# Kernel tuning notes

Hardware: AMD Instinct MI355X
Metric: run time of the kernel (lower is better)

## Reference

```python
import jax, jax.numpy as jnp
import numpy as np

N_ENT = 50000
N_REL2 = 100   # num_relations * 2
N_BASES = 16
DIM = 64
N_EDGES = 100000


def _rgcn_conv(x, edge_index, edge_type, edge_norm, basis, att, root, bias):
    # x: [N, D]; basis: [B, D, D]; att: [R, B]; root: [D, D]; bias: [D]
    src = edge_index[0]
    dst = edge_index[1]
    num_nodes = x.shape[0]
    # Per-edge relation weight is w[edge_type] with w = att @ basis (reshaped).
    # By linearity we contract x_j with each basis first, then mix with the
    # per-edge attention coefficients -- same math, avoids the [E, D, D] gather.
    coeff = att[edge_type]                          # [E, B]
    xb = jnp.einsum('ei,bio->ebo', x[src], basis)   # [E, B, D]
    msg = jnp.einsum('eb,ebo->eo', coeff, xb)       # [E, D]
    msg = msg * edge_norm[:, None]
    # scatter-mean aggregation at target nodes
    s = jax.ops.segment_sum(msg, dst, num_segments=num_nodes)
    cnt = jax.ops.segment_sum(jnp.ones((msg.shape[0],), msg.dtype), dst,
                              num_segments=num_nodes)
    agg = s / jnp.maximum(cnt, 1.0)[:, None]
    # root transform + bias
    return agg + x @ root + bias


def setup_inputs() -> dict:
    key = jax.random.key(0)
    ks = jax.random.split(key, 12)
    E = N_EDGES
    inp = {
        'entity': jnp.arange(N_ENT, dtype=jnp.int64) if jax.config.jax_enable_x64 else jnp.arange(N_ENT, dtype=jnp.int32),
        'edge_index': jax.random.randint(ks[0], (2, E), 0, N_ENT),
        'edge_type': jax.random.randint(ks[1], (E,), 0, N_REL2),
        'edge_norm': jax.random.uniform(ks[2], (E,), dtype=jnp.float32),
        'emb': jax.random.normal(ks[3], (N_ENT, DIM), dtype=jnp.float32) * 0.1,
        'basis1': jax.random.normal(ks[4], (N_BASES, DIM, DIM), dtype=jnp.float32) * 0.05,
        'att1': jax.random.normal(ks[5], (N_REL2, N_BASES), dtype=jnp.float32) * 0.1,
        'root1': jax.random.normal(ks[6], (DIM, DIM), dtype=jnp.float32) * 0.05,
        'bias1': jnp.zeros((DIM,), dtype=jnp.float32),
        'basis2': jax.random.normal(ks[7], (N_BASES, DIM, DIM), dtype=jnp.float32) * 0.05,
        'att2': jax.random.normal(ks[8], (N_REL2, N_BASES), dtype=jnp.float32) * 0.1,
        'root2': jax.random.normal(ks[9], (DIM, DIM), dtype=jnp.float32) * 0.05,
        'bias2': jnp.zeros((DIM,), dtype=jnp.float32),
    }
    return inp


def reference(entity, edge_index, edge_type, edge_norm, emb,
              basis1, att1, root1, bias1, basis2, att2, root2, bias2):
    x = emb[entity]                                  # embedding lookup [N, D]
    x = _rgcn_conv(x, edge_index, edge_type, edge_norm, basis1, att1, root1, bias1)
    x = _rgcn_conv(x, edge_index, edge_type, edge_norm, basis2, att2, root2, bias2)
    return x
```

## Files before the change

kernel.cpp:

```cpp
#include <hip/hip_runtime.h>

#define NN 50000
#define NR 100
#define NB 16
#define D  64
#define NE 100000

#define HB  196
#define EPB 512
#define ZB  196
#define GB  ((NN * 16 + 255) / 256)

#define CHUNK 128
#define GROUPS 2
#define EGRID 1024

#define NPB 128
#define NGRID ((NN + NPB - 1) / NPB)

typedef float f32x4  __attribute__((ext_vector_type(4)));
typedef short bf16x8 __attribute__((ext_vector_type(8)));

__device__ __forceinline__ short f2bf(float f) {
    unsigned u = __float_as_uint(f);
    return (short)((u + 0x7FFFu + ((u >> 16) & 1u)) >> 16);
}

__device__ __forceinline__ bf16x8 pack8(f32x4 a, f32x4 b) {
    bf16x8 t;
    t[0] = f2bf(a.x); t[1] = f2bf(a.y); t[2] = f2bf(a.z); t[3] = f2bf(a.w);
    t[4] = f2bf(b.x); t[5] = f2bf(b.y); t[6] = f2bf(b.z); t[7] = f2bf(b.w);
    return t;
}

__global__ __launch_bounds__(256) void prep_all(
    const float* __restrict__ att1, const float* __restrict__ basis1,
    const float* __restrict__ root1,
    const float* __restrict__ att2, const float* __restrict__ basis2,
    const float* __restrict__ root2,
    const int* __restrict__ entity, const f32x4* __restrict__ emb4,
    float* __restrict__ Wt1, float* __restrict__ Wt2,
    float* __restrict__ rT1, float* __restrict__ rT2,
    f32x4* __restrict__ x04, int* __restrict__ deg, int* __restrict__ nodeCur)
{
    __shared__ float t[64 * 65];
    int b = blockIdx.x;
    if (b < 2 * NR) {
        int layer = b >= NR;
        int r = layer ? b - NR : b;
        const float* att   = layer ? att2 : att1;
        const float* basis = layer ? basis2 : basis1;
        float*       Wt    = layer ? Wt2 : Wt1;
        float a[NB];
#pragma unroll
        for (int bb = 0; bb < NB; ++bb) a[bb] = att[r * NB + bb];
#pragma unroll
        for (int i = 0; i < 16; ++i) {
            int idx = i * 256 + threadIdx.x;
            float acc = 0.f;
#pragma unroll
            for (int bb = 0; bb < NB; ++bb) acc += a[bb] * basis[bb * 4096 + idx];
            t[(idx >> 6) * 65 + (idx & 63)] = acc;
        }
        __syncthreads();
#pragma unroll
        for (int i = 0; i < 16; ++i) {
            int j = i * 256 + threadIdx.x;
            Wt[(size_t)r * 4096 + j] = t[(j & 63) * 65 + (j >> 6)];
        }
    } else if (b < 2 * NR + 2) {
        const float* root = (b == 2 * NR) ? root1 : root2;
        float*       rT   = (b == 2 * NR) ? rT1 : rT2;
#pragma unroll
        for (int i = 0; i < 16; ++i) {
            int idx = i * 256 + threadIdx.x;
            t[(idx >> 6) * 65 + (idx & 63)] = root[idx];
        }
        __syncthreads();
#pragma unroll
        for (int i = 0; i < 16; ++i) {
            int j = i * 256 + threadIdx.x;
            rT[j] = t[(j & 63) * 65 + (j >> 6)];
        }
    } else if (b < 2 * NR + 2 + ZB) {
        int i = (b - (2 * NR + 2)) * 256 + threadIdx.x;
        deg[i] = 0; nodeCur[i] = 0;
    } else {
        int idx = (b - (2 * NR + 2 + ZB)) * 256 + threadIdx.x;
        if (idx < NN * 16) {
            int n = idx >> 4;
            int q = idx & 15;
            x04[idx] = emb4[(size_t)entity[n] * 16 + q];
        }
    }
}

__global__ __launch_bounds__(256) void hist_edges(
    const int* __restrict__ et, const int* __restrict__ dst,
    int* __restrict__ blockHist, int* __restrict__ deg)
{
    __shared__ int lh[NR];
    for (int i = threadIdx.x; i < NR; i += 256) lh[i] = 0;
    __syncthreads();
#pragma unroll
    for (int i = 0; i < EPB / 256; ++i) {
        int e = blockIdx.x * EPB + i * 256 + threadIdx.x;
        if (e < NE) {
            atomicAdd(&lh[et[e]], 1);
            atomicAdd(&deg[dst[e]], 1);
        }
    }
    __syncthreads();
    for (int i = threadIdx.x; i < NR; i += 256)
        blockHist[blockIdx.x * NR + i] = lh[i];
}

__global__ __launch_bounds__(256) void scans(
    const int* __restrict__ blockHist, int* __restrict__ blockPrefix,
    int* __restrict__ relTot, const int* __restrict__ deg,
    int* __restrict__ nodePre, int* __restrict__ blockSumN)
{
    __shared__ int sc[256];
    int t = threadIdx.x;
    if (blockIdx.x < NR) {
        int r = blockIdx.x;
        int v = (t < HB) ? blockHist[t * NR + r] : 0;
        sc[t] = v;
        __syncthreads();
#pragma unroll
        for (int off = 1; off < 256; off <<= 1) {
            int a = (t >= off) ? sc[t - off] : 0;
            __syncthreads();
            sc[t] += a;
            __syncthreads();
        }
        if (t < HB) blockPrefix[t * NR + r] = sc[t] - v;
        if (t == 0) relTot[r] = sc[255];
    } else {
        int b = blockIdx.x - NR;
        int n = b * 256 + t;
        int v = deg[n];
        sc[t] = v;
        __syncthreads();
#pragma unroll
        for (int off = 1; off < 256; off <<= 1) {
            int a = (t >= off) ? sc[t - off] : 0;
            __syncthreads();
            sc[t] += a;
            __syncthreads();
        }
        nodePre[n] = sc[t] - v;
        if (t == 255) blockSumN[b] = sc[255];
    }
}

__global__ __launch_bounds__(256) void scanK(
    const int* __restrict__ relTot, const int* __restrict__ blockSumN,
    int* __restrict__ offs, int* __restrict__ nbG,
    int* __restrict__ tabR, int* __restrict__ tabS,
    int* __restrict__ nodeBlockBase)
{
    __shared__ int totL[NR];
    __shared__ int offL[NR + 1];
    __shared__ int cnbL[NR + 1];
    __shared__ int sc2[256];
    int t = threadIdx.x;
    if (t < NR) totL[t] = relTot[t];
    int v2 = (t < ZB) ? blockSumN[t] : 0;
    sc2[t] = v2;
    __syncthreads();
    if (t == 0) {
        int off = 0, cb = 0;
        for (int r = 0; r < NR; ++r) {
            offL[r] = off; cnbL[r] = cb;
            off += totL[r];
            cb  += (totL[r] + CHUNK - 1) / CHUNK;
        }
        offL[NR] = off; cnbL[NR] = cb;
    }
    __syncthreads();
#pragma unroll
    for (int off = 1; off < 256; off <<= 1) {
        int a = (t >= off) ? sc2[t - off] : 0;
        __syncthreads();
        sc2[t] += a;
        __syncthreads();
    }
    if (t < ZB) nodeBlockBase[t] = sc2[t] - v2;
    if (t == 0) nodeBlockBase[ZB] = sc2[255];
    if (t <= NR) offs[t] = offL[t];
    if (t == 0) nbG[0] = cnbL[NR];
    int nb = cnbL[NR];
    for (int e = t; e < nb; e += 256) {
        int lo = 0, hi = NR;
        while (hi - lo > 1) { int mid = (lo + hi) >> 1; if (cnbL[mid] <= e) lo = mid; else hi = mid; }
        tabR[e] = lo;
        tabS[e] = offL[lo] + (e - cnbL[lo]) * CHUNK;
    }
}

__global__ __launch_bounds__(256) void scatter2(
    const int* __restrict__ src, const int* __restrict__ dst,
    const int* __restrict__ et, const float* __restrict__ en,
    const int* __restrict__ offs, const int* __restrict__ blockPrefix,
    const int* __restrict__ nodePre, const int* __restrict__ nodeBlockBase,
    int* __restrict__ nodeCur, int* __restrict__ srcS,
    float* __restrict__ normS, int* __restrict__ dstIdx)
{
    __shared__ int lcur[NR];
    for (int i = threadIdx.x; i < NR; i += 256)
        lcur[i] = offs[i] + blockPrefix[blockIdx.x * NR + i];
    __syncthreads();
#pragma unroll
    for (int i = 0; i < EPB / 256; ++i) {
        int e = blockIdx.x * EPB + i * 256 + threadIdx.x;
        if (e < NE) {
            int r = et[e];
            int p = atomicAdd(&lcur[r], 1);
            srcS[p] = src[e]; normS[p] = en[e];
            int n = dst[e];
            int q = nodeBlockBase[n >> 8] + nodePre[n] + atomicAdd(&nodeCur[n], 1);
            dstIdx[q] = p;
        }
    }
}

__global__ __launch_bounds__(256, 4) void edge_mfma(
    const int* __restrict__ srcS, const float* __restrict__ normS,
    const int* __restrict__ offs, const int* __restrict__ tabR,
    const int* __restrict__ tabS, const int* __restrict__ nbG,
    const float* __restrict__ x, const float* __restrict__ Wt,
    float* __restrict__ msg)
{
    __shared__ float LW[64 * 68];
    int b = blockIdx.x;
    if (b >= nbG[0]) return;
    int r  = tabR[b];
    int cs = tabS[b];
    int tid = threadIdx.x;

    {
        const f32x4* __restrict__ Wg = (const f32x4*)(Wt + (size_t)r * 4096);
#pragma unroll
        for (int i = 0; i < 4; ++i) {
            int v = tid + i * 256;
            int d = v >> 4, k4 = v & 15;
            *(f32x4*)(LW + d * 68 + k4 * 4) = Wg[v];
        }
    }
    __syncthreads();

    int lane = tid & 63, wid = tid >> 6;
    int c15 = lane & 15, kg = lane >> 4;

    bf16x8 B[4][2];
#pragma unroll
    for (int nt = 0; nt < 4; ++nt)
#pragma unroll
        for (int ks = 0; ks < 2; ++ks) {
            const f32x4* p = (const f32x4*)(LW + (nt * 16 + c15) * 68 + ks * 32 + kg * 8);
            B[nt][ks] = pack8(p[0], p[1]);
        }

    int segE = offs[r + 1];
    int bend = cs + CHUNK < segE ? cs + CHUNK : segE;

#pragma unroll 1
    for (int g = 0; g < GROUPS; ++g) {
        int gs = cs + wid * (GROUPS * 16) + g * 16;
        if (gs >= bend) break;
        int ge = gs + 16 < bend ? gs + 16 : bend;

        int e  = gs + c15;
        int ec = e < ge ? e : ge - 1;
        float nrm = (e < ge) ? normS[ec] : 0.f;
        int   sn  = srcS[ec];

        const f32x4* xr  = (const f32x4*)(x + (size_t)sn * 64 + kg * 8);
        const f32x4* xr2 = (const f32x4*)(x + (size_t)sn * 64 + 32 + kg * 8);
        bf16x8 A0 = pack8(xr[0]  * nrm, xr[1]  * nrm);
        bf16x8 A1 = pack8(xr2[0] * nrm, xr2[1] * nrm);

        f32x4 z = {0.f, 0.f, 0.f, 0.f};
        f32x4 acc[4] = {z, z, z, z};
#pragma unroll
        for (int nt = 0; nt < 4; ++nt) {
            acc[nt] = __builtin_amdgcn_mfma_f32_16x16x32_bf16(A0, B[nt][0], acc[nt], 0, 0, 0);
            acc[nt] = __builtin_amdgcn_mfma_f32_16x16x32_bf16(A1, B[nt][1], acc[nt], 0, 0, 0);
        }
#pragma unroll
        for (int nt = 0; nt < 4; ++nt)
#pragma unroll
            for (int j = 0; j < 4; ++j) {
                int er = gs + kg * 4 + j;
                if (er < ge)
                    msg[(size_t)er * 64 + nt * 16 + c15] = acc[nt][j];
            }
    }
}

__global__ __launch_bounds__(256) void agg_mean(
    const float* __restrict__ msg, const int* __restrict__ dstIdx,
    const int* __restrict__ nodePre, const int* __restrict__ nodeBB,
    float* __restrict__ agg)
{
    int n    = blockIdx.x * 4 + (threadIdx.x >> 6);
    int lane = threadIdx.x & 63;
    if (n >= NN) return;
    int blk  = n >> 8;
    int base = nodeBB[blk];
    int lo = base + nodePre[n];
    int hi = ((n & 255) == 255) ? nodeBB[blk + 1] : base + nodePre[n + 1];
    float acc = 0.f;
    for (int q = lo; q < hi; ++q)
        acc += msg[(size_t)dstIdx[q] * 64 + lane];
    float c = (float)(hi - lo);
    c = c > 1.f ? c : 1.f;
    agg[(size_t)n * 64 + lane] = acc / c;
}

__global__ __launch_bounds__(256, 4) void node_mfma(
    const float* __restrict__ x, const float* __restrict__ agg,
    const float* __restrict__ rT, const float* __restrict__ bias,
    float* __restrict__ out)
{
    __shared__ float LW[64 * 68];
    int tid = threadIdx.x;
    {
        const f32x4* __restrict__ Rg = (const f32x4*)rT;
#pragma unroll
        for (int i = 0; i < 4; ++i) {
            int v = tid + i * 256;
            int d = v >> 4, k4 = v & 15;
            *(f32x4*)(LW + d * 68 + k4 * 4) = Rg[v];
        }
    }
    __syncthreads();

    int lane = tid & 63, wid = tid >> 6;
    int c15 = lane & 15, kg = lane >> 4;

    bf16x8 B[4][2];
#pragma unroll
    for (int nt = 0; nt < 4; ++nt)
#pragma unroll
        for (int ks = 0; ks < 2; ++ks) {
            const f32x4* p = (const f32x4*)(LW + (nt * 16 + c15) * 68 + ks * 32 + kg * 8);
            B[nt][ks] = pack8(p[0], p[1]);
        }
    float bv[4];
#pragma unroll
    for (int nt = 0; nt < 4; ++nt) bv[nt] = bias[nt * 16 + c15];

#pragma unroll 1
    for (int g = 0; g < GROUPS; ++g) {
        int gs = blockIdx.x * NPB + wid * (GROUPS * 16) + g * 16;
        if (gs >= NN) break;
        int ge = gs + 16 < NN ? gs + 16 : NN;

        int n  = gs + c15;
        int nc = n < ge ? n : ge - 1;
        const f32x4* xr  = (const f32x4*)(x + (size_t)nc * 64 + kg * 8);
        const f32x4* xr2 = (const f32x4*)(x + (size_t)nc * 64 + 32 + kg * 8);
        bf16x8 A0 = pack8(xr[0], xr[1]);
        bf16x8 A1 = pack8(xr2[0], xr2[1]);

        f32x4 z = {0.f, 0.f, 0.f, 0.f};
        f32x4 acc[4] = {z, z, z, z};
#pragma unroll
        for (int nt = 0; nt < 4; ++nt) {
            acc[nt] = __builtin_amdgcn_mfma_f32_16x16x32_bf16(A0, B[nt][0], acc[nt], 0, 0, 0);
            acc[nt] = __builtin_amdgcn_mfma_f32_16x16x32_bf16(A1, B[nt][1], acc[nt], 0, 0, 0);
        }
#pragma unroll
        for (int nt = 0; nt < 4; ++nt)
#pragma unroll
            for (int j = 0; j < 4; ++j) {
                int nr = gs + kg * 4 + j;
                if (nr < ge) {
                    size_t off = (size_t)nr * 64 + nt * 16 + c15;
                    out[off] = agg[off] + acc[nt][j] + bv[nt];
                }
            }
    }
}

extern "C" void kernel_launch(void* const* d_in, const int* in_sizes, int n_in,
                              void* d_out, int out_size, void* d_ws, size_t ws_size,
                              hipStream_t stream) {
    const int*   entity    = (const int*)d_in[0];
    const int*   edge_index= (const int*)d_in[1];
    const int*   edge_type = (const int*)d_in[2];
    const float* edge_norm = (const float*)d_in[3];
    const float* emb       = (const float*)d_in[4];
    const float* basis1    = (const float*)d_in[5];
    const float* att1      = (const float*)d_in[6];
    const float* root1     = (const float*)d_in[7];
    const float* bias1     = (const float*)d_in[8];
    const float* basis2    = (const float*)d_in[9];
    const float* att2      = (const float*)d_in[10];
    const float* root2     = (const float*)d_in[11];
    const float* bias2     = (const float*)d_in[12];

    const int* src = edge_index;
    const int* dst = edge_index + NE;

    float* ws    = (float*)d_ws;
    float* Wt1   = ws;
    float* Wt2   = Wt1 + (size_t)NR * 4096;
    float* rT1   = Wt2 + (size_t)NR * 4096;
    float* rT2   = rT1 + 4096;
    float* x0    = rT2 + 4096;
    float* msg   = x0  + (size_t)NN * D;
    float* agg   = msg + (size_t)NE * D;
    float* normS = agg + (size_t)NN * D;
    int*   offs        = (int*)(normS + NE);
    int*   relTot      = offs + NR + 3;
    int*   nbG         = relTot + NR;
    int*   blockHist   = nbG + 3;
    int*   blockPrefix = blockHist + HB * NR;
    int*   tabR        = blockPrefix + HB * NR;
    int*   tabS        = tabR + EGRID;
    int*   srcS        = tabS + EGRID;
    int*   deg         = srcS + NE;
    int*   nodePre     = deg + ZB * 256;
    int*   nodeCur     = nodePre + ZB * 256;
    int*   blockSumN   = nodeCur + ZB * 256;
    int*   nodeBB      = blockSumN + ZB + 4;
    int*   dstIdx      = nodeBB + ZB + 5;

    float* out = (float*)d_out;

    prep_all<<<2 * NR + 2 + ZB + GB, 256, 0, stream>>>(
        att1, basis1, root1, att2, basis2, root2,
        entity, (const f32x4*)emb, Wt1, Wt2, rT1, rT2,
        (f32x4*)x0, deg, nodeCur);
    hist_edges<<<HB, 256, 0, stream>>>(edge_type, dst, blockHist, deg);
    scans<<<NR + ZB, 256, 0, stream>>>(blockHist, blockPrefix, relTot,
                                       deg, nodePre, blockSumN);
    scanK<<<1, 256, 0, stream>>>(relTot, blockSumN, offs, nbG, tabR, tabS, nodeBB);
    scatter2<<<HB, 256, 0, stream>>>(src, dst, edge_type, edge_norm,
                                     offs, blockPrefix, nodePre, nodeBB,
                                     nodeCur, srcS, normS, dstIdx);

    edge_mfma<<<EGRID, 256, 0, stream>>>(srcS, normS, offs, tabR, tabS, nbG,
                                         x0, Wt1, msg);
    agg_mean<<<(NN + 3) / 4, 256, 0, stream>>>(msg, dstIdx, nodePre, nodeBB, agg);
    node_mfma<<<NGRID, 256, 0, stream>>>(x0, agg, rT1, bias1, out);

    edge_mfma<<<EGRID, 256, 0, stream>>>(srcS, normS, offs, tabR, tabS, nbG,
                                         out, Wt2, msg);
    agg_mean<<<(NN + 3) / 4, 256, 0, stream>>>(msg, dstIdx, nodePre, nodeBB, agg);
    node_mfma<<<NGRID, 256, 0, stream>>>(out, agg, rT2, bias2, out);
}
```

Baseline: 128.5 us.

## Pad relation segments to 16, load weights per wave, fuse aggregation with node transform

Each relation's edge segment is padded to a multiple of 16 with zero-norm dummy edges, and a per-edge relation id array is stored. Every 16-edge MFMA group therefore has a single relation, which removes the chunk lookup tables. The edge kernel reads the relation id per group and loads its weights straight from global memory into registers, dropping the LDS staging and block barrier. The mean aggregation and root-transform kernels are merged into one agg_node kernel per layer, cutting two launches. The cost is padded msg rows plus repeated global weight reads per wave that hit L2.

```diff
diff --git a/kernel.cpp b/kernel.cpp
--- a/kernel.cpp
+++ b/kernel.cpp
@@ -5,18 +5,19 @@
 #define NB 16
 #define D  64
 #define NE 100000
+#define NE2 (NE + 16 * NR)
 
 #define HB  196
 #define EPB 512
 #define ZB  196
 #define GB  ((NN * 16 + 255) / 256)
 
-#define CHUNK 128
 #define GROUPS 2
-#define EGRID 1024
-
-#define NPB 128
-#define NGRID ((NN + NPB - 1) / NPB)
+#define EPBK (64 * GROUPS)
+#define EGRID ((NE2 + EPBK - 1) / EPBK)
+
+#define NPBK 64
+#define NGRID ((NN + NPBK - 1) / NPBK)
 
 typedef float f32x4  __attribute__((ext_vector_type(4)));
 typedef short bf16x8 __attribute__((ext_vector_type(8)));
@@ -156,13 +157,11 @@
 
 __global__ __launch_bounds__(256) void scanK(
     const int* __restrict__ relTot, const int* __restrict__ blockSumN,
-    int* __restrict__ offs, int* __restrict__ nbG,
-    int* __restrict__ tabR, int* __restrict__ tabS,
-    int* __restrict__ nodeBlockBase)
+    int* __restrict__ offs, int* __restrict__ nbG, int* __restrict__ nodeBB,
+    int* __restrict__ srcS, float* __restrict__ normS, int* __restrict__ rS)
 {
     __shared__ int totL[NR];
     __shared__ int offL[NR + 1];
-    __shared__ int cnbL[NR + 1];
     __shared__ int sc2[256];
     int t = threadIdx.x;
     if (t < NR) totL[t] = relTot[t];
@@ -170,13 +169,12 @@
     sc2[t] = v2;
     __syncthreads();
     if (t == 0) {
-        int off = 0, cb = 0;
+        int off = 0;
         for (int r = 0; r < NR; ++r) {
-            offL[r] = off; cnbL[r] = cb;
-            off += totL[r];
-            cb  += (totL[r] + CHUNK - 1) / CHUNK;
-        }
-        offL[NR] = off; cnbL[NR] = cb;
+            offL[r] = off;
+            off = (off + totL[r] + 15) & ~15;
+        }
+        offL[NR] = off;
     }
     __syncthreads();
 #pragma unroll
@@ -186,16 +184,13 @@
         sc2[t] += a;
         __syncthreads();
     }
-    if (t < ZB) nodeBlockBase[t] = sc2[t] - v2;
-    if (t == 0) nodeBlockBase[ZB] = sc2[255];
+    if (t < ZB) nodeBB[t] = sc2[t] - v2;
+    if (t == 0) nodeBB[ZB] = sc2[255];
     if (t <= NR) offs[t] = offL[t];
-    if (t == 0) nbG[0] = cnbL[NR];
-    int nb = cnbL[NR];
-    for (int e = t; e < nb; e += 256) {
-        int lo = 0, hi = NR;
-        while (hi - lo > 1) { int mid = (lo + hi) >> 1; if (cnbL[mid] <= e) lo = mid; else hi = mid; }
-        tabR[e] = lo;
-        tabS[e] = offL[lo] + (e - cnbL[lo]) * CHUNK;
+    if (t == 0) nbG[0] = offL[NR];
+    if (t < NR) {
+        int g0 = offL[t] + totL[t], g1 = offL[t + 1];
+        for (int p = g0; p < g1; ++p) { srcS[p] = 0; normS[p] = 0.f; rS[p] = t; }
     }
 }
 
@@ -205,7 +200,7 @@
     const int* __restrict__ offs, const int* __restrict__ blockPrefix,
     const int* __restrict__ nodePre, const int* __restrict__ nodeBlockBase,
     int* __restrict__ nodeCur, int* __restrict__ srcS,
-    float* __restrict__ normS, int* __restrict__ dstIdx)
+    float* __restrict__ normS, int* __restrict__ rS, int* __restrict__ dstIdx)
 {
     __shared__ int lcur[NR];
     for (int i = threadIdx.x; i < NR; i += 256)
@@ -217,7 +212,7 @@
         if (e < NE) {
             int r = et[e];
             int p = atomicAdd(&lcur[r], 1);
-            srcS[p] = src[e]; normS[p] = en[e];
+            srcS[p] = src[e]; normS[p] = en[e]; rS[p] = r;
             int n = dst[e];
             int q = nodeBlockBase[n >> 8] + nodePre[n] + atomicAdd(&nodeCur[n], 1);
             dstIdx[q] = p;
@@ -225,57 +220,38 @@
     }
 }
 
-__global__ __launch_bounds__(256, 4) void edge_mfma(
+__global__ __launch_bounds__(256) void edge_mfma(
     const int* __restrict__ srcS, const float* __restrict__ normS,
-    const int* __restrict__ offs, const int* __restrict__ tabR,
-    const int* __restrict__ tabS, const int* __restrict__ nbG,
+    const int* __restrict__ rS, const int* __restrict__ nbG,
     const float* __restrict__ x, const float* __restrict__ Wt,
     float* __restrict__ msg)
 {
-    __shared__ float LW[64 * 68];
-    int b = blockIdx.x;
-    if (b >= nbG[0]) return;
-    int r  = tabR[b];
-    int cs = tabS[b];
     int tid = threadIdx.x;
-
-    {
-        const f32x4* __restrict__ Wg = (const f32x4*)(Wt + (size_t)r * 4096);
-#pragma unroll
-        for (int i = 0; i < 4; ++i) {
-            int v = tid + i * 256;
-            int d = v >> 4, k4 = v & 15;
-            *(f32x4*)(LW + d * 68 + k4 * 4) = Wg[v];
-        }
-    }
-    __syncthreads();
-
     int lane = tid & 63, wid = tid >> 6;
     int c15 = lane & 15, kg = lane >> 4;
-
+    int padTot = nbG[0];
+    int rcur = -1;
     bf16x8 B[4][2];
-#pragma unroll
-    for (int nt = 0; nt < 4; ++nt)
-#pragma unroll
-        for (int ks = 0; ks < 2; ++ks) {
-            const f32x4* p = (const f32x4*)(LW + (nt * 16 + c15) * 68 + ks * 32 + kg * 8);
-            B[nt][ks] = pack8(p[0], p[1]);
-        }
-
-    int segE = offs[r + 1];
-    int bend = cs + CHUNK < segE ? cs + CHUNK : segE;
 
 #pragma unroll 1
     for (int g = 0; g < GROUPS; ++g) {
-        int gs = cs + wid * (GROUPS * 16) + g * 16;
-        if (gs >= bend) break;
-        int ge = gs + 16 < bend ? gs + 16 : bend;
-
+        int gs = blockIdx.x * EPBK + wid * (16 * GROUPS) + g * 16;
+        if (gs >= padTot) break;
+        int r = __builtin_amdgcn_readfirstlane(rS[gs]);
+        if (r != rcur) {
+            rcur = r;
+            const float* __restrict__ Wr = Wt + (size_t)r * 4096;
+#pragma unroll
+            for (int nt = 0; nt < 4; ++nt)
+#pragma unroll
+                for (int ks = 0; ks < 2; ++ks) {
+                    const f32x4* p = (const f32x4*)(Wr + (nt * 16 + c15) * 64 + ks * 32 + kg * 8);
+                    B[nt][ks] = pack8(p[0], p[1]);
+                }
+        }
         int e  = gs + c15;
-        int ec = e < ge ? e : ge - 1;
-        float nrm = (e < ge) ? normS[ec] : 0.f;
-        int   sn  = srcS[ec];
-
+        float nrm = normS[e];
+        int   sn  = srcS[e];
         const f32x4* xr  = (const f32x4*)(x + (size_t)sn * 64 + kg * 8);
         const f32x4* xr2 = (const f32x4*)(x + (size_t)sn * 64 + 32 + kg * 8);
         bf16x8 A0 = pack8(xr[0]  * nrm, xr[1]  * nrm);
@@ -291,98 +267,79 @@
 #pragma unroll
         for (int nt = 0; nt < 4; ++nt)
 #pragma unroll
-            for (int j = 0; j < 4; ++j) {
-                int er = gs + kg * 4 + j;
-                if (er < ge)
-                    msg[(size_t)er * 64 + nt * 16 + c15] = acc[nt][j];
-            }
-    }
-}
-
-__global__ __launch_bounds__(256) void agg_mean(
-    const float* __restrict__ msg, const int* __restrict__ dstIdx,
-    const int* __restrict__ nodePre, const int* __restrict__ nodeBB,
-    float* __restrict__ agg)
-{
-    int n    = blockIdx.x * 4 + (threadIdx.x >> 6);
-    int lane = threadIdx.x & 63;
-    if (n >= NN) return;
-    int blk  = n >> 8;
-    int base = nodeBB[blk];
-    int lo = base + nodePre[n];
-    int hi = ((n & 255) == 255) ? nodeBB[blk + 1] : base + nodePre[n + 1];
-    float acc = 0.f;
-    for (int q = lo; q < hi; ++q)
-        acc += msg[(size_t)dstIdx[q] * 64 + lane];
-    float c = (float)(hi - lo);
-    c = c > 1.f ? c : 1.f;
-    agg[(size_t)n * 64 + lane] = acc / c;
-}
-
-__global__ __launch_bounds__(256, 4) void node_mfma(
-    const float* __restrict__ x, const float* __restrict__ agg,
-    const float* __restrict__ rT, const float* __restrict__ bias,
+            for (int j = 0; j < 4; ++j)
+                msg[(size_t)(gs + kg * 4 + j) * 64 + nt * 16 + c15] = acc[nt][j];
+    }
+}
+
+__global__ __launch_bounds__(256) void agg_node(
+    const float* __restrict__ x, const float* __restrict__ msg,
+    const int* __restrict__ dstIdx, const int* __restrict__ nodePre,
+    const int* __restrict__ nodeBB, const float* __restrict__ rT,
+    const float* __restrict__ bias, float* __restrict__ agg,
     float* __restrict__ out)
 {
-    __shared__ float LW[64 * 68];
     int tid = threadIdx.x;
-    {
-        const f32x4* __restrict__ Rg = (const f32x4*)rT;
-#pragma unroll
-        for (int i = 0; i < 4; ++i) {
-            int v = tid + i * 256;
-            int d = v >> 4, k4 = v & 15;
-            *(f32x4*)(LW + d * 68 + k4 * 4) = Rg[v];
-        }
-    }
-    __syncthreads();
-
     int lane = tid & 63, wid = tid >> 6;
     int c15 = lane & 15, kg = lane >> 4;
+    int wbase = blockIdx.x * NPBK + wid * 16;
+
+#pragma unroll 1
+    for (int ln = 0; ln < 16; ++ln) {
+        int n = wbase + ln;
+        if (n >= NN) break;
+        int blk  = n >> 8;
+        int base = nodeBB[blk];
+        int lo = base + nodePre[n];
+        int hi = ((n & 255) == 255) ? nodeBB[blk + 1] : base + nodePre[n + 1];
+        float acc = 0.f;
+        for (int q = lo; q < hi; ++q)
+            acc += msg[(size_t)dstIdx[q] * 64 + lane];
+        float c = (float)(hi - lo);
+        c = c > 1.f ? c : 1.f;
+        agg[(size_t)n * 64 + lane] = acc / c;
+    }
+    __syncthreads();
+
+    if (wbase >= NN) return;
+    int ge = wbase + 16 < NN ? wbase + 16 : NN;
 
     bf16x8 B[4][2];
 #pragma unroll
     for (int nt = 0; nt < 4; ++nt)
 #pragma unroll
         for (int ks = 0; ks < 2; ++ks) {
-            const f32x4* p = (const f32x4*)(LW + (nt * 16 + c15) * 68 + ks * 32 + kg * 8);
+            const f32x4* p = (const f32x4*)(rT + (nt * 16 + c15) * 64 + ks * 32 + kg * 8);
             B[nt][ks] = pack8(p[0], p[1]);
         }
     float bv[4];
 #pragma unroll
     for (int nt = 0; nt < 4; ++nt) bv[nt] = bias[nt * 16 + c15];
 
-#pragma unroll 1
-    for (int g = 0; g < GROUPS; ++g) {
-        int gs = blockIdx.x * NPB + wid * (GROUPS * 16) + g * 16;
-        if (gs >= NN) break;
-        int ge = gs + 16 < NN ? gs + 16 : NN;
-
-        int n  = gs + c15;
-        int nc = n < ge ? n : ge - 1;
-        const f32x4* xr  = (const f32x4*)(x + (size_t)nc * 64 + kg * 8);
-        const f32x4* xr2 = (const f32x4*)(x + (size_t)nc * 64 + 32 + kg * 8);
-        bf16x8 A0 = pack8(xr[0], xr[1]);
-        bf16x8 A1 = pack8(xr2[0], xr2[1]);
-
-        f32x4 z = {0.f, 0.f, 0.f, 0.f};
-        f32x4 acc[4] = {z, z, z, z};
-#pragma unroll
-        for (int nt = 0; nt < 4; ++nt) {
-            acc[nt] = __builtin_amdgcn_mfma_f32_16x16x32_bf16(A0, B[nt][0], acc[nt], 0, 0, 0);
-            acc[nt] = __builtin_amdgcn_mfma_f32_16x16x32_bf16(A1, B[nt][1], acc[nt], 0, 0, 0);
-        }
-#pragma unroll
-        for (int nt = 0; nt < 4; ++nt)
-#pragma unroll
-            for (int j = 0; j < 4; ++j) {
-                int nr = gs + kg * 4 + j;
-                if (nr < ge) {
-                    size_t off = (size_t)nr * 64 + nt * 16 + c15;
-                    out[off] = agg[off] + acc[nt][j] + bv[nt];
-                }
+    int n  = wbase + c15;
+    int nc = n < ge ? n : ge - 1;
+    const f32x4* xr  = (const f32x4*)(x + (size_t)nc * 64 + kg * 8);
+    const f32x4* xr2 = (const f32x4*)(x + (size_t)nc * 64 + 32 + kg * 8);
+    bf16x8 A0 = pack8(xr[0], xr[1]);
+    bf16x8 A1 = pack8(xr2[0], xr2[1]);
+
+    f32x4 z = {0.f, 0.f, 0.f, 0.f};
+    f32x4 acc[4] = {z, z, z, z};
+#pragma unroll
+    for (int nt = 0; nt < 4; ++nt) {
+        acc[nt] = __builtin_amdgcn_mfma_f32_16x16x32_bf16(A0, B[nt][0], acc[nt], 0, 0, 0);
+        acc[nt] = __builtin_amdgcn_mfma_f32_16x16x32_bf16(A1, B[nt][1], acc[nt], 0, 0, 0);
+    }
+#pragma unroll
+    for (int nt = 0; nt < 4; ++nt)
+#pragma unroll
+        for (int j = 0; j < 4; ++j) {
+            int nr = wbase + kg * 4 + j;
+            if (nr < ge) {
+                size_t off = (size_t)nr * 64 + nt * 16 + c15;
+                out[off] = agg[off] + acc[nt][j] + bv[nt];
             }
-    }
+        }
 }
 
 extern "C" void kernel_launch(void* const* d_in, const int* in_sizes, int n_in,
@@ -412,17 +369,16 @@
     float* rT2   = rT1 + 4096;
     float* x0    = rT2 + 4096;
     float* msg   = x0  + (size_t)NN * D;
-    float* agg   = msg + (size_t)NE * D;
+    float* agg   = msg + (size_t)NE2 * D;
     float* normS = agg + (size_t)NN * D;
-    int*   offs        = (int*)(normS + NE);
+    int*   offs        = (int*)(normS + NE2);
     int*   relTot      = offs + NR + 3;
     int*   nbG         = relTot + NR;
     int*   blockHist   = nbG + 3;
     int*   blockPrefix = blockHist + HB * NR;
-    int*   tabR        = blockPrefix + HB * NR;
-    int*   tabS        = tabR + EGRID;
-    int*   srcS        = tabS + EGRID;
-    int*   deg         = srcS + NE;
+    int*   srcS        = blockPrefix + HB * NR;
+    int*   rS          = srcS + NE2;
+    int*   deg         = rS + NE2;
     int*   nodePre     = deg + ZB * 256;
     int*   nodeCur     = nodePre + ZB * 256;
     int*   blockSumN   = nodeCur + ZB * 256;
@@ -438,18 +394,17 @@
     hist_edges<<<HB, 256, 0, stream>>>(edge_type, dst, blockHist, deg);
     scans<<<NR + ZB, 256, 0, stream>>>(blockHist, blockPrefix, relTot,
                                        deg, nodePre, blockSumN);
-    scanK<<<1, 256, 0, stream>>>(relTot, blockSumN, offs, nbG, tabR, tabS, nodeBB);
+    scanK<<<1, 256, 0, stream>>>(relTot, blockSumN, offs, nbG, nodeBB,
+                                 srcS, normS, rS);
     scatter2<<<HB, 256, 0, stream>>>(src, dst, edge_type, edge_norm,
                                      offs, blockPrefix, nodePre, nodeBB,
-                                     nodeCur, srcS, normS, dstIdx);
-
-    edge_mfma<<<EGRID, 256, 0, stream>>>(srcS, normS, offs, tabR, tabS, nbG,
-                                         x0, Wt1, msg);
-    agg_mean<<<(NN + 3) / 4, 256, 0, stream>>>(msg, dstIdx, nodePre, nodeBB, agg);
-    node_mfma<<<NGRID, 256, 0, stream>>>(x0, agg, rT1, bias1, out);
-
-    edge_mfma<<<EGRID, 256, 0, stream>>>(srcS, normS, offs, tabR, tabS, nbG,
-                                         out, Wt2, msg);
-    agg_mean<<<(NN + 3) / 4, 256, 0, stream>>>(msg, dstIdx, nodePre, nodeBB, agg);
-    node_mfma<<<NGRID, 256, 0, stream>>>(out, agg, rT2, bias2, out);
-}
+                                     nodeCur, srcS, normS, rS, dstIdx);
+
+    edge_mfma<<<EGRID, 256, 0, stream>>>(srcS, normS, rS, nbG, x0, Wt1, msg);
+    agg_node<<<NGRID, 256, 0, stream>>>(x0, msg, dstIdx, nodePre, nodeBB,
+                                        rT1, bias1, agg, out);
+
+    edge_mfma<<<EGRID, 256, 0, stream>>>(srcS, normS, rS, nbG, out, Wt2, msg);
+    agg_node<<<NGRID, 256, 0, stream>>>(out, msg, dstIdx, nodePre, nodeBB,
+                                        rT2, bias2, agg, out);
+}
```

Result: slower. 155.9 us (+21.4%).
